# Performance work log

Hardware: AMD Instinct MI355X
Metric: run time of the kernel (lower is better)

Reference implementation:

```python
import jax, jax.numpy as jnp
import numpy as np

B, S, HID = 2, 1024, 2048
NH, HD = 16, 128          # num_heads, head_dim
NN = 16                   # num_neighbors
RHID = 1024               # hidden_size // compression_factor
CTX = 2                   # context_size
SCALE = HD ** -0.5


def setup_inputs() -> dict:
    key = jax.random.key(0)
    ks = jax.random.split(key, 6)
    return {
        "hidden_states": jax.random.normal(ks[0], (B, S, HID), jnp.float32),
        "ext_hidden_states": jax.random.normal(ks[1], (B, S, NN, RHID), jnp.float32),
        # weights stored (in_features, out_features)
        "Wq": jax.random.normal(ks[2], (HID, NH * HD), jnp.float32) * 0.02,
        "Wk": jax.random.normal(ks[3], (RHID, NH * HD), jnp.float32) * 0.02,
        "Wv": jax.random.normal(ks[4], (RHID, NH * HD), jnp.float32) * 0.02,
        "Wo": jax.random.normal(ks[5], (NH * HD, HID), jnp.float32) * 0.02,
    }


def _repeat_neighbors(n, seq_len):
    # n: [B, S, H, NN, HD] -> [B, S, H, CTX*NN, HD], gathering a ctx window
    # of previous positions' neighbors for each query (clamped at 0).
    context = jnp.clip(
        jnp.arange(seq_len)[:, None] + jnp.arange(-CTX + 1, 1)[None, :],
        0, seq_len - 1)                     # [S, CTX]
    n = jnp.moveaxis(n, 1, 2)               # [B, H, S, NN, HD]
    n = n[:, :, context]                    # [B, H, S, CTX, NN, HD]
    n = n.reshape(n.shape[0], n.shape[1], seq_len, -1, HD)
    return jnp.moveaxis(n, 1, 2)            # [B, S, H, CTX*NN, HD]


def reference(hidden_states, ext_hidden_states, Wq, Wk, Wv, Wo):
    b, s, hid = hidden_states.shape
    nn_ = ext_hidden_states.shape[2]
    q = (hidden_states @ Wq) * SCALE
    q = q.reshape(b, s, NH, HD)                         # [B,S,H,D]
    # note: original views [B,S,NN,H*D] as [B,S,H,NN,D] (pure reshape)
    k = (ext_hidden_states @ Wk).reshape(b, s, NH, nn_, HD)
    v = (ext_hidden_states @ Wv).reshape(b, s, NH, nn_, HD)
    if CTX > 1:
        k = _repeat_neighbors(k, s)                     # [B,S,H,I,D]
        v = _repeat_neighbors(v, s)
    attn = jnp.einsum('bqhd,bqhid->bhqi', q, k)
    attn = jax.nn.softmax(attn.astype(jnp.float32), axis=-1).astype(q.dtype)
    out = jnp.einsum('bhqi,bqhid->bqhd', attn, v)
    out = out.reshape(b, s, hid) @ Wo
    return out + hidden_states
```

## Files before the change

### kernel.cpp

```cpp
#include <hip/hip_runtime.h>
#include <stdint.h>

#define DEVI __device__ __forceinline__

typedef __bf16 bf16x8 __attribute__((ext_vector_type(8)));
typedef float f32x4 __attribute__((ext_vector_type(4)));
typedef unsigned short u16;

static constexpr float SCALE_ = 0.08838834764831845f;

DEVI u16 f2bf(float f) {
  uint32_t u = __float_as_uint(f);
  u += 0x7fffu + ((u >> 16) & 1u);
  return (u16)(u >> 16);
}
DEVI float bfraw2f(uint32_t hi) { return __uint_as_float(hi); }

__global__ void k_cast(const float* __restrict__ in, u16* __restrict__ out) {
  int i = blockIdx.x * blockDim.x + threadIdx.x;
  float4 v = ((const float4*)in)[i];
  ushort4 o;
  o.x = f2bf(v.x); o.y = f2bf(v.y); o.z = f2bf(v.z); o.w = f2bf(v.w);
  ((ushort4*)out)[i] = o;
}

__global__ void k_transpose_cast(const float* __restrict__ in, u16* __restrict__ out,
                                 int R, int C) {
  __shared__ float t[32][33];
  int tx = threadIdx.x & 31, ty = threadIdx.x >> 5;
  int c0 = blockIdx.x << 5, r0 = blockIdx.y << 5;
  #pragma unroll
  for (int rr = 0; rr < 32; rr += 8) t[ty + rr][tx] = in[(r0 + ty + rr) * C + c0 + tx];
  __syncthreads();
  #pragma unroll
  for (int rr = 0; rr < 32; rr += 8) out[(c0 + ty + rr) * R + r0 + tx] = f2bf(t[tx][ty + rr]);
}

DEVI void gl_lds16(const u16* g, u16* l) {
  __builtin_amdgcn_global_load_lds((const __attribute__((address_space(1))) void*)g,
                                   (__attribute__((address_space(3))) void*)l, 16, 0, 0);
}

template<bool OUTF32, bool RESID>
__global__ __launch_bounds__(256, 2) void k_gemm(
    const u16* __restrict__ A, const u16* __restrict__ Bt, void* __restrict__ Cv,
    const float* __restrict__ resid, int M, int N, int K, float scale) {
  __shared__ __align__(16) u16 As[128 * 32];
  __shared__ __align__(16) u16 Bs[128 * 32];
  const int nbn = N >> 7;
  const int bm = blockIdx.x / nbn, bn = blockIdx.x - bm * nbn;
  const int tid = threadIdx.x, w = tid >> 6, lane = tid & 63;
  const int wr = w >> 1, wc = w & 1;
  const int lr = lane & 15, kg = lane >> 4;

  const u16* Ab = A + (size_t)bm * 128 * K;
  const u16* Bb = Bt + (size_t)bn * 128 * K;

  f32x4 acc[4][4] = {};

  for (int k0 = 0; k0 < K; k0 += 32) {
    #pragma unroll
    for (int t = 0; t < 2; t++) {
      const int ub = w * 128 + t * 64;
      const int u = ub + lane;
      const size_t go = (size_t)(u >> 2) * K + k0 + (u & 3) * 8;
      gl_lds16(Ab + go, &As[ub * 8]);
      gl_lds16(Bb + go, &Bs[ub * 8]);
    }
    __syncthreads();
    bf16x8 af[4], bv[4];
    #pragma unroll
    for (int m = 0; m < 4; m++) af[m] = *(const bf16x8*)&As[(wr * 64 + m * 16 + lr) * 32 + kg * 8];
    #pragma unroll
    for (int n = 0; n < 4; n++) bv[n] = *(const bf16x8*)&Bs[(wc * 64 + n * 16 + lr) * 32 + kg * 8];
    #pragma unroll
    for (int m = 0; m < 4; m++)
      #pragma unroll
      for (int n = 0; n < 4; n++)
        acc[m][n] = __builtin_amdgcn_mfma_f32_16x16x32_bf16(af[m], bv[n], acc[m][n], 0, 0, 0);
    __syncthreads();
  }

  const int r0 = bm * 128 + wr * 64 + kg * 4;
  const int c0 = bn * 128 + wc * 64 + lr;
  #pragma unroll
  for (int m = 0; m < 4; m++)
    #pragma unroll
    for (int n = 0; n < 4; n++)
      #pragma unroll
      for (int j = 0; j < 4; j++) {
        size_t idx = (size_t)(r0 + m * 16 + j) * N + (c0 + n * 16);
        float v = acc[m][n][j] * scale;
        if constexpr (OUTF32) {
          if constexpr (RESID) v += resid[idx];
          ((float*)Cv)[idx] = v;
        } else {
          ((u16*)Cv)[idx] = f2bf(v);
        }
      }
}

__global__ __launch_bounds__(512, 2) void k_kv256(
    const u16* __restrict__ A, const u16* __restrict__ Bt, u16* __restrict__ C) {
  constexpr int K = 1024, NT = K / 64, LDC = 4096;
  __shared__ __align__(16) u16 lds[65536];
  char* ldsc = (char*)lds;
  const int tid = threadIdx.x, w = tid >> 6, lane = tid & 63;
  const int wr = w >> 2, wc = w & 3;
  const int lr = lane & 15, kg = lane >> 4, x3 = lr & 7;
  const int bm = blockIdx.x >> 4, bn = blockIdx.x & 15;

  const int u0 = tid, u1 = 512 + tid;
  const int r0s = u0 >> 3, r1s = u1 >> 3;
  const int ro0 = r0s * K + ((u0 & 7) ^ (r0s & 7)) * 8;
  const int ro1 = r1s * K + ((u1 & 7) ^ (r1s & 7)) * 8;
  const u16* Ab = A + (size_t)bm * 256 * K;
  const u16* Bb = Bt + (size_t)bn * 256 * K;

  auto stage = [&](int db2, int q, int k64) {
    const int h = q & 1;
    const u16* base = (q >= 2) ? Bb : Ab;
    uint32_t dst = ((q >= 2) ? 65536u : 0u) + (uint32_t)(db2 * 2 + h) * 16384u
                   + (uint32_t)w * 1024u;
    const size_t tb = (size_t)h * 128 * K + k64;
    gl_lds16(base + tb + ro0, (u16*)(ldsc + dst));
    gl_lds16(base + tb + ro1, (u16*)(ldsc + dst + 8192u));
  };

  f32x4 acc[8][4] = {};

  #pragma unroll
  for (int q = 0; q < 4; ++q) stage(0, q, 0);
  __builtin_amdgcn_sched_barrier(0);

  for (int kt = 0; kt < NT; ++kt) {
    const int c = kt & 1;
    const int nk64 = (kt + 1 < NT ? kt + 1 : kt) * 64;
    __builtin_amdgcn_sched_barrier(0);
    __builtin_amdgcn_s_barrier();
    __builtin_amdgcn_sched_barrier(0);
    stage(c ^ 1, 0, nk64);
    __builtin_amdgcn_sched_barrier(0);
    asm volatile("s_waitcnt vmcnt(2)" ::: "memory");
    __builtin_amdgcn_sched_barrier(0);
    __builtin_amdgcn_s_barrier();
    __builtin_amdgcn_sched_barrier(0);

    const uint32_t a_base = (uint32_t)(c * 2 + wr) * 16384u;
    const uint32_t b_base = 65536u + (uint32_t)(c * 2 + (wc >> 1)) * 16384u;
    #pragma unroll
    for (int q = 0; q < 4; ++q) {
      if (q > 0) { stage(c ^ 1, q, nk64); __builtin_amdgcn_sched_barrier(0); }
      const int mh = q >> 1, nh = q & 1;
      bf16x8 af[4][2], bfr[2][2];
      #pragma unroll
      for (int m = 0; m < 4; ++m)
        #pragma unroll
        for (int ks = 0; ks < 2; ++ks)
          af[m][ks] = *(const bf16x8*)(ldsc + a_base + (mh * 64 + m * 16 + lr) * 128
                                       + ((((ks << 2) | kg) ^ x3) << 4));
      #pragma unroll
      for (int n = 0; n < 2; ++n)
        #pragma unroll
        for (int ks = 0; ks < 2; ++ks)
          bfr[n][ks] = *(const bf16x8*)(ldsc + b_base
                                        + ((wc & 1) * 64 + (nh * 2 + n) * 16 + lr) * 128
                                        + ((((ks << 2) | kg) ^ x3) << 4));
      __builtin_amdgcn_s_setprio(1);
      #pragma unroll
      for (int m = 0; m < 4; ++m)
        #pragma unroll
        for (int n = 0; n < 2; ++n)
          #pragma unroll
          for (int ks = 0; ks < 2; ++ks)
            acc[mh * 4 + m][nh * 2 + n] = __builtin_amdgcn_mfma_f32_16x16x32_bf16(
                af[m][ks], bfr[n][ks], acc[mh * 4 + m][nh * 2 + n], 0, 0, 0);
      __builtin_amdgcn_s_setprio(0);
    }
  }

  const int gr0 = bm * 256 + wr * 128 + kg * 4;
  const int gc0 = bn * 256 + wc * 64 + lr;
  #pragma unroll
  for (int m = 0; m < 8; ++m)
    #pragma unroll
    for (int n = 0; n < 4; ++n)
      #pragma unroll
      for (int j = 0; j < 4; ++j)
        C[(size_t)(gr0 + m * 16 + j) * LDC + gc0 + n * 16] = f2bf(acc[m][n][j]);
}

__global__ __launch_bounds__(128, 2) void k_attn(
    const u16* __restrict__ Q, const u16* __restrict__ KV, u16* __restrict__ O) {
  __shared__ __align__(16) u16 Kl[2][32][136];
  __shared__ __align__(16) u16 Vl[2][32][136];
  __shared__ __align__(16) u16 ql[2 * 128];
  const int tid = threadIdx.x;
  const int hg = blockIdx.x & 7;
  const int s = blockIdx.x >> 3;
  const int sm1 = s ? s - 1 : 0;

  #pragma unroll
  for (int it = 0; it < 8; it++) {
    int e = (it * 128 + tid) * 8;
    int hh = e >> 12;
    int rem = e & 4095;
    int ifull = rem >> 7, d = rem & 127;
    int ctx = ifull >> 4, i = ifull & 15;
    int h = hg * 2 + hh;
    size_t g = ((size_t)(ctx ? s : sm1) * 16 + h) * 4096 + i * 128 + d;
    *(bf16x8*)&Kl[hh][ifull][d] = *(const bf16x8*)&KV[g];
    *(bf16x8*)&Vl[hh][ifull][d] = *(const bf16x8*)&KV[g + 2048];
  }
  if (tid < 32) *(bf16x8*)&ql[tid * 8] = *(const bf16x8*)&Q[(size_t)s * 2048 + hg * 256 + tid * 8];
  __syncthreads();

  const int w = tid >> 6, lane = tid & 63;
  const int ni = lane & 31, dh = lane >> 5;
  float sc = 0.f;
  #pragma unroll
  for (int t = 0; t < 8; t++) {
    bf16x8 kv = *(const bf16x8*)&Kl[w][ni][dh * 64 + t * 8];
    bf16x8 qv = *(const bf16x8*)&ql[w * 128 + dh * 64 + t * 8];
    #pragma unroll
    for (int j = 0; j < 8; j++) sc += (float)kv[j] * (float)qv[j];
  }
  sc += __shfl_xor(sc, 32);
  float mx = sc;
  #pragma unroll
  for (int m_ = 16; m_; m_ >>= 1) mx = fmaxf(mx, __shfl_xor(mx, m_));
  float ex = __expf(sc - mx);
  float sm = ex;
  #pragma unroll
  for (int m_ = 16; m_; m_ >>= 1) sm += __shfl_xor(sm, m_);
  float pr = ex / sm;

  float o0 = 0.f, o1 = 0.f;
  #pragma unroll
  for (int i2 = 0; i2 < 32; i2++) {
    float pi = __shfl(pr, i2);
    uint32_t vv = *(const uint32_t*)&Vl[w][i2][lane * 2];
    o0 += pi * bfraw2f(vv << 16);
    o1 += pi * bfraw2f(vv & 0xffff0000u);
  }
  int h = hg * 2 + w;
  uint32_t ov = (uint32_t)f2bf(o0) | ((uint32_t)f2bf(o1) << 16);
  *(uint32_t*)&O[((size_t)s * 16 + h) * 128 + lane * 2] = ov;
}

extern "C" void kernel_launch(void* const* d_in, const int* in_sizes, int n_in,
                              void* d_out, int out_size, void* d_ws, size_t ws_size,
                              hipStream_t stream) {
  (void)in_sizes; (void)n_in; (void)out_size; (void)ws_size;
  const float* hs  = (const float*)d_in[0];
  const float* ext = (const float*)d_in[1];
  const float* Wq  = (const float*)d_in[2];
  const float* Wk  = (const float*)d_in[3];
  const float* Wv  = (const float*)d_in[4];
  const float* Wo  = (const float*)d_in[5];
  float* out = (float*)d_out;

  char* p = (char*)d_ws;
  auto alloc = [&](size_t elems) {
    u16* r = (u16*)p;
    p += ((elems * 2 + 255) & ~(size_t)255);
    return r;
  };
  u16* hs_bf  = alloc(4ull << 20);
  u16* ext_bf = alloc(32ull << 20);
  u16* Wq_t   = alloc(4ull << 20);
  u16* Wkv_t  = alloc(8ull << 20);
  u16* Wo_t   = alloc(4ull << 20);
  u16* Qb     = alloc(4ull << 20);
  u16* KVbuf  = alloc(64ull << 20);
  u16* Ob     = hs_bf;

  k_cast<<<4096, 256, 0, stream>>>(hs, hs_bf);
  k_cast<<<32768, 256, 0, stream>>>(ext, ext_bf);
  k_transpose_cast<<<dim3(64, 64), 256, 0, stream>>>(Wq, Wq_t, 2048, 2048);
  k_transpose_cast<<<dim3(64, 32), 256, 0, stream>>>(Wk, Wkv_t, 1024, 2048);
  k_transpose_cast<<<dim3(64, 32), 256, 0, stream>>>(Wv, Wkv_t + (2048ull * 1024), 1024, 2048);
  k_transpose_cast<<<dim3(64, 64), 256, 0, stream>>>(Wo, Wo_t, 2048, 2048);

  k_gemm<false, false><<<256, 256, 0, stream>>>(hs_bf, Wq_t, Qb, nullptr,
                                                2048, 2048, 2048, SCALE_);
  for (int b = 0; b < 2; b++) {
    const u16* extb = ext_bf + (size_t)b * 16384 * 1024;
    k_kv256<<<64 * 16, 512, 0, stream>>>(extb, Wkv_t, KVbuf);
    k_attn<<<1024 * 8, 128, 0, stream>>>(Qb + (size_t)b * 1024 * 2048, KVbuf,
                                         Ob + (size_t)b * 1024 * 2048);
  }
  k_gemm<true, true><<<256, 256, 0, stream>>>(Ob, Wo_t, out, hs,
                                              2048, 2048, 2048, 1.0f);
}
```

Measured before the change: 651.9 us.

## Merge cast/transpose launches and restructure kv256 staging barriers

Merges the two fp32-to-bf16 cast launches into one kernel and the four weight transpose-cast launches into one kernel that picks its source by blockIdx.y, removing per-launch overhead. In the 256-tile kernel's main loop, the leading barrier is dropped and each quarter-stage prefetch is issued after the LDS fragment reads, with extra barriers and an lgkmcnt wait around every MFMA group. This should let each sub-buffer be overwritten safely as soon as it has been read, but it adds several block-wide barriers per k-step, which may reduce overlap between loads and MFMAs.

Result: slower. 700.4 us (+7.4%).

```diff
diff --git a/kernel.cpp b/kernel.cpp
--- a/kernel.cpp
+++ b/kernel.cpp
@@ -16,19 +16,36 @@
 }
 DEVI float bfraw2f(uint32_t hi) { return __uint_as_float(hi); }
 
-__global__ void k_cast(const float* __restrict__ in, u16* __restrict__ out) {
+__global__ void k_cast2(const float* __restrict__ a, u16* __restrict__ ao, int na4,
+                        const float* __restrict__ b, u16* __restrict__ bo) {
   int i = blockIdx.x * blockDim.x + threadIdx.x;
-  float4 v = ((const float4*)in)[i];
+  const float* src;
+  u16* dst;
+  int j;
+  if (i < na4) { src = a; dst = ao; j = i; }
+  else { src = b; dst = bo; j = i - na4; }
+  float4 v = ((const float4*)src)[j];
   ushort4 o;
   o.x = f2bf(v.x); o.y = f2bf(v.y); o.z = f2bf(v.z); o.w = f2bf(v.w);
-  ((ushort4*)out)[i] = o;
-}
-
-__global__ void k_transpose_cast(const float* __restrict__ in, u16* __restrict__ out,
-                                 int R, int C) {
+  ((ushort4*)dst)[j] = o;
+}
+
+__global__ void k_tc4(const float* __restrict__ Wq, u16* __restrict__ Wq_t,
+                      const float* __restrict__ Wk, const float* __restrict__ Wv,
+                      u16* __restrict__ Wkv_t, const float* __restrict__ Wo,
+                      u16* __restrict__ Wo_t) {
   __shared__ float t[32][33];
+  const float* in;
+  u16* out;
+  int R, yb;
+  int y = blockIdx.y;
+  if (y < 64) { in = Wq; out = Wq_t; R = 2048; yb = 0; }
+  else if (y < 96) { in = Wk; out = Wkv_t; R = 1024; yb = 64; }
+  else if (y < 128) { in = Wv; out = Wkv_t + (2048ull * 1024); R = 1024; yb = 96; }
+  else { in = Wo; out = Wo_t; R = 2048; yb = 128; }
+  const int C = 2048;
   int tx = threadIdx.x & 31, ty = threadIdx.x >> 5;
-  int c0 = blockIdx.x << 5, r0 = blockIdx.y << 5;
+  int c0 = blockIdx.x << 5, r0 = (y - yb) << 5;
   #pragma unroll
   for (int rr = 0; rr < 32; rr += 8) t[ty + rr][tx] = in[(r0 + ty + rr) * C + c0 + tx];
   __syncthreads();
@@ -133,24 +150,20 @@
   for (int q = 0; q < 4; ++q) stage(0, q, 0);
   __builtin_amdgcn_sched_barrier(0);
 
-  for (int kt = 0; kt < NT; ++kt) {
-    const int c = kt & 1;
-    const int nk64 = (kt + 1 < NT ? kt + 1 : kt) * 64;
-    __builtin_amdgcn_sched_barrier(0);
-    __builtin_amdgcn_s_barrier();
-    __builtin_amdgcn_sched_barrier(0);
-    stage(c ^ 1, 0, nk64);
+  for (int t = 0; t < NT; ++t) {
+    const int d = t & 1;
+    const int nk64 = (t + 1 < NT ? t + 1 : t) * 64;
+    stage(d ^ 1, 0, nk64);
     __builtin_amdgcn_sched_barrier(0);
     asm volatile("s_waitcnt vmcnt(2)" ::: "memory");
     __builtin_amdgcn_sched_barrier(0);
     __builtin_amdgcn_s_barrier();
     __builtin_amdgcn_sched_barrier(0);
 
-    const uint32_t a_base = (uint32_t)(c * 2 + wr) * 16384u;
-    const uint32_t b_base = 65536u + (uint32_t)(c * 2 + (wc >> 1)) * 16384u;
+    const uint32_t a_base = (uint32_t)(d * 2 + wr) * 16384u;
+    const uint32_t b_base = 65536u + (uint32_t)(d * 2 + (wc >> 1)) * 16384u;
     #pragma unroll
     for (int q = 0; q < 4; ++q) {
-      if (q > 0) { stage(c ^ 1, q, nk64); __builtin_amdgcn_sched_barrier(0); }
       const int mh = q >> 1, nh = q & 1;
       bf16x8 af[4][2], bfr[2][2];
       #pragma unroll
@@ -166,6 +179,11 @@
           bfr[n][ks] = *(const bf16x8*)(ldsc + b_base
                                         + ((wc & 1) * 64 + (nh * 2 + n) * 16 + lr) * 128
                                         + ((((ks << 2) | kg) ^ x3) << 4));
+      if (q < 3) stage(d ^ 1, q + 1, nk64);
+      __builtin_amdgcn_sched_barrier(0);
+      __builtin_amdgcn_s_barrier();
+      asm volatile("s_waitcnt lgkmcnt(0)" ::: "memory");
+      __builtin_amdgcn_sched_barrier(0);
       __builtin_amdgcn_s_setprio(1);
       #pragma unroll
       for (int m = 0; m < 4; ++m)
@@ -176,6 +194,8 @@
             acc[mh * 4 + m][nh * 2 + n] = __builtin_amdgcn_mfma_f32_16x16x32_bf16(
                 af[m][ks], bfr[n][ks], acc[mh * 4 + m][nh * 2 + n], 0, 0, 0);
       __builtin_amdgcn_s_setprio(0);
+      __builtin_amdgcn_sched_barrier(0);
+      __builtin_amdgcn_s_barrier();
     }
   }
 
@@ -275,12 +295,8 @@
   u16* KVbuf  = alloc(64ull << 20);
   u16* Ob     = hs_bf;
 
-  k_cast<<<4096, 256, 0, stream>>>(hs, hs_bf);
-  k_cast<<<32768, 256, 0, stream>>>(ext, ext_bf);
-  k_transpose_cast<<<dim3(64, 64), 256, 0, stream>>>(Wq, Wq_t, 2048, 2048);
-  k_transpose_cast<<<dim3(64, 32), 256, 0, stream>>>(Wk, Wkv_t, 1024, 2048);
-  k_transpose_cast<<<dim3(64, 32), 256, 0, stream>>>(Wv, Wkv_t + (2048ull * 1024), 1024, 2048);
-  k_transpose_cast<<<dim3(64, 64), 256, 0, stream>>>(Wo, Wo_t, 2048, 2048);
+  k_cast2<<<36864, 256, 0, stream>>>(hs, hs_bf, 1048576, ext, ext_bf);
+  k_tc4<<<dim3(64, 192), 256, 0, stream>>>(Wq, Wq_t, Wk, Wv, Wkv_t, Wo, Wo_t);
 
   k_gemm<false, false><<<256, 256, 0, stream>>>(hs_bf, Wq_t, Qb, nullptr,
                                                 2048, 2048, 2048, SCALE_);
```
